# Kernel tuning notes

Hardware: AMD Instinct MI355X
Metric: run time of the kernel (lower is better)

## Reference

```python
import jax, jax.numpy as jnp
import numpy as np
from functools import partial

H, W = 96, 96                 # PNet output feature-map size
N = H * W                     # candidate boxes
STRIDE = 2.0
CELL = 12.0
SCALE = 12.0 / 20.0           # net_size / min_face_size (first pyramid level)
CLS_THR = 0.6
NMS_THR1 = 0.5                # per-scale NMS
NMS_THR2 = 0.7                # final NMS


def _iou_matrix(b):
    # b: [N,4] boxes (x1,y1,x2,y2); pixel convention with +1, eps as in source
    x1, y1, x2, y2 = b[:, 0], b[:, 1], b[:, 2], b[:, 3]
    area = (x2 - x1 + 1.0) * (y2 - y1 + 1.0)                      # [N]
    xx1 = jnp.maximum(x1[:, None], x1[None, :])
    yy1 = jnp.maximum(y1[:, None], y1[None, :])
    xx2 = jnp.minimum(x2[:, None], x2[None, :])
    yy2 = jnp.minimum(y2[:, None], y2[None, :])
    w = jnp.maximum(0.0, xx2 - xx1 + 1.0)
    h = jnp.maximum(0.0, yy2 - yy1 + 1.0)
    inter = w * h                                                  # [N,N]
    return inter / (area[:, None] + area[None, :] - inter + 1e-10)


def _greedy_nms(iou, valid, thr):
    # Sequential greedy suppression over score-sorted boxes (rows of iou).
    # A kept box suppresses all LOWER-ranked boxes with IoU > thr.
    n = valid.shape[0]
    ranks = jnp.arange(n)

    def step(suppressed, i):
        kept_i = valid[i] & (~suppressed[i])
        suppressed = suppressed | (kept_i & (iou[i] > thr) & (ranks > i))
        return suppressed, kept_i

    _, keep = jax.lax.scan(step, jnp.zeros(n, dtype=bool), ranks)
    return keep


def _forward(cls_map, reg):
    score = cls_map.reshape(-1)                                    # [N]
    dreg = reg.reshape(-1, 4)                                      # [N,4]
    ys, xs = jnp.meshgrid(jnp.arange(H, dtype=cls_map.dtype),
                          jnp.arange(W, dtype=cls_map.dtype), indexing='ij')
    x1 = jnp.round(STRIDE * xs / SCALE).reshape(-1)
    y1 = jnp.round(STRIDE * ys / SCALE).reshape(-1)
    x2 = jnp.round((STRIDE * xs + CELL) / SCALE).reshape(-1)
    y2 = jnp.round((STRIDE * ys + CELL) / SCALE).reshape(-1)
    boxes = jnp.stack([x1, y1, x2, y2], axis=1)                    # [N,4]

    order = jnp.argsort(-score)                                    # desc by score
    b = boxes[order]
    s = score[order]
    d = dreg[order]
    valid = s > CLS_THR                                            # threshold-gather as mask

    iou = _iou_matrix(b)                                           # [N,N] ~340MB
    keep = _greedy_nms(iou, valid, NMS_THR1)                       # per-scale NMS
    keep = _greedy_nms(iou, keep, NMS_THR2)                        # final NMS

    # box calibration (boxes_c in the source)
    bbw = b[:, 2] - b[:, 0] + 1.0
    bbh = b[:, 3] - b[:, 1] + 1.0
    boxes_c = jnp.stack([b[:, 0] + d[:, 0] * bbw,
                         b[:, 1] + d[:, 1] * bbh,
                         b[:, 2] + d[:, 2] * bbw,
                         b[:, 3] + d[:, 3] * bbh,
                         s], axis=1)                               # [N,5]
    return boxes_c * keep[:, None].astype(boxes_c.dtype)


def setup_inputs() -> dict:
    key = jax.random.key(0)
    k1, k2 = jax.random.split(key)
    cls_map = jax.random.uniform(k1, (H, W), dtype=jnp.float32)        # face prob channel
    reg = 0.1 * jax.random.normal(k2, (H, W, 4), dtype=jnp.float32)    # bbox offsets
    return {"cls_map": cls_map, "reg": reg}


def reference(cls_map, reg):
    return _forward(cls_map, reg)
```

## Files before the change

### kernel.cpp

```cpp
#include <hip/hip_runtime.h>
#include <stdint.h>

#define HH 96
#define WW 96
#define NN (HH*WW)
#define NW 192
#define NMT 24
#define MT 384
#define NKT 9


__device__ __forceinline__ int coord1(int a) { return (10 * a + 1) / 3; }

__device__ __forceinline__ unsigned long long shifted(unsigned long long A,
                                                      unsigned long long B,
                                                      int h, int dj) {
    const unsigned long long W0 = h ? B : A;
    if (dj == 0) return W0;
    if (dj > 0) {
        const unsigned long long Wr = h ? 0ULL : B;
        return (W0 >> dj) | (Wr << (64 - dj));
    }
    const int d = -dj;
    const unsigned long long Wl = h ? A : 0ULL;
    return (W0 << d) | (Wl >> (64 - d));
}

__global__ __launch_bounds__(1024, 1) void kA(const float* __restrict__ cls,
                                              unsigned int* __restrict__ rankp,
                                              unsigned long long* __restrict__ kw) {
    __shared__ __align__(16) float s[NN];
    __shared__ unsigned long long Hh[12][NW];
    __shared__ unsigned long long K[NW], D[NW];
    const int tid = threadIdx.x;
    const int bid = blockIdx.x;

    if (bid != 0) {
        const int rb = bid - 1;
        const int kt = rb % NKT, mt = rb / NKT;
        const int base = mt * MT;
        unsigned long long* sk = (unsigned long long*)s;
        if (tid < MT) {
            const int m = base + tid;
            sk[tid] = ((unsigned long long)__float_as_uint(cls[m]) << 14)
                    | (unsigned long long)(16383 - m);
        }
        __syncthreads();
        const int k = kt * 1024 + tid;
        const unsigned long long kk =
            ((unsigned long long)__float_as_uint(cls[k]) << 14)
          | (unsigned long long)(16383 - k);
        const ulonglong2* sk2 = (const ulonglong2*)sk;
        unsigned c0 = 0, c1 = 0;
        #pragma unroll 4
        for (int m2 = 0; m2 < MT / 2; ++m2) {
            const ulonglong2 v = sk2[m2];
            c0 += (v.x > kk);
            c1 += (v.y > kk);
        }
        rankp[mt * NN + k] = c0 + c1;
        return;
    }

    const int lane = tid & 63;
    const int wave = tid >> 6;
    const int offs_di[12] = {0,0, 0,0, -1,1, -2,2, -1,-1, 1,1};
    const int offs_dj[12] = {-1,1,-2,2,  0,0,  0,0, -1, 1,-1,1};
    for (int i = tid; i < NN/4; i += 1024)
        ((float4*)s)[i] = ((const float4*)cls)[i];
    __syncthreads();
    for (int it = 0; it < 12; ++it) {
        const int w = wave + (it << 4);
        const int row = w >> 1;
        const int col = ((w & 1) << 6) + lane;
        const bool incell = (col < WW);
        const int c = row * WW + col;
        const float sc = incell ? s[c] : 0.0f;
        const unsigned bc = __float_as_uint(sc);
        const int cm3 = col % 3, rm3 = row % 3;
        const unsigned long long dinit = __ballot(!incell || !(sc > 0.6f));
        if (lane == 0) { D[w] = dinit; K[w] = 0ULL; }
        #pragma unroll
        for (int e = 0; e < 12; ++e) {
            const int ii = row + offs_di[e], jj = col + offs_dj[e];
            bool geo;
            switch (e) {
                case 2:  geo = (cm3 == 1); break;
                case 3:  geo = (cm3 == 2); break;
                case 6:  geo = (rm3 == 1); break;
                case 7:  geo = (rm3 == 2); break;
                case 8:  geo = !(cm3 == 2 && rm3 == 2); break;
                case 9:  geo = !(cm3 == 1 && rm3 == 2); break;
                case 10: geo = !(cm3 == 2 && rm3 == 1); break;
                case 11: geo = !(cm3 == 1 && rm3 == 1); break;
                default: geo = true;
            }
            const bool tb = (e==0)|(e==2)|(e==4)|(e==6)|(e==8)|(e==9);
            bool hp = false;
            if (incell && geo && ii >= 0 && ii < HH && jj >= 0 && jj < WW) {
                const unsigned bv = __float_as_uint(s[ii * WW + jj]);
                hp = tb ? (bv >= bc) : (bv > bc);
            }
            const unsigned long long m = __ballot(hp);
            if (lane == 0) Hh[e][w] = m;
        }
    }
    __syncthreads();
    if (wave >= 3) return;

    volatile unsigned long long* vK = K;
    volatile unsigned long long* vD = D;
    const int w = tid;
    const int row = w >> 1, h = w & 1;
    unsigned long long Hr[12];
    #pragma unroll
    for (int e = 0; e < 12; ++e) Hr[e] = Hh[e][w];
    unsigned long long myK = K[w], myD = D[w];
    for (int iter = 0; iter < 4096; ++iter) {
        if (!~myD) break;
        unsigned long long DA[5], DB[5], KA[5], KB[5];
        #pragma unroll
        for (int q = 0; q < 5; ++q) {
            const int rr = row + q - 2;
            const bool ok = (rr >= 0) && (rr < HH);
            DA[q] = ok ? vD[rr*2]   : 0ULL;
            DB[q] = ok ? vD[rr*2+1] : 0ULL;
        }
        #pragma unroll
        for (int q = 0; q < 5; ++q) {
            const int rr = row + q - 2;
            const bool ok = (rr >= 0) && (rr < HH);
            KA[q] = ok ? vK[rr*2]   : 0ULL;
            KB[q] = ok ? vK[rr*2+1] : 0ULL;
        }
        unsigned long long supp = 0ULL, alldet = ~0ULL;
        #pragma unroll
        for (int e = 0; e < 12; ++e) {
            const int q = offs_di[e] + 2;
            const int dj = offs_dj[e];
            supp   |=  Hr[e] & shifted(KA[q], KB[q], h, dj);
            alldet &= ~Hr[e] | shifted(DA[q], DB[q], h, dj);
        }
        const unsigned long long U = ~myD;
        myK = myK | (U & alldet & ~supp);
        myD = myD | (U & (supp | alldet));
        vK[w] = myK;
        vD[w] = myD;
    }
    kw[w] = myK;
}

__global__ void kout(const float* __restrict__ score, const float* __restrict__ reg,
                     const unsigned int* __restrict__ rankp,
                     const unsigned long long* __restrict__ kw,
                     float* __restrict__ out) {
    const int k = blockIdx.x * 256 + threadIdx.x;
    unsigned r = 0;
    #pragma unroll
    for (int y = 0; y < NMT; ++y) r += rankp[y * NN + k];
    const int j = k % WW, i = k / WW;
    const bool kp = ((kw[i * 2 + (j >> 6)] >> (j & 63)) & 1ULL) != 0ULL;
    const float x1 = (float)coord1(j);
    const float y1 = (float)coord1(i);
    const float4 d = ((const float4*)reg)[k];
    float* o = out + (size_t)r * 5;
    o[0] = kp ? (x1 + d.x * 21.0f) : 0.0f;
    o[1] = kp ? (y1 + d.y * 21.0f) : 0.0f;
    o[2] = kp ? (x1 + 20.0f + d.z * 21.0f) : 0.0f;
    o[3] = kp ? (y1 + 20.0f + d.w * 21.0f) : 0.0f;
    o[4] = kp ? score[k] : 0.0f;
}

extern "C" void kernel_launch(void* const* d_in, const int* in_sizes, int n_in,
                              void* d_out, int out_size, void* d_ws, size_t ws_size,
                              hipStream_t stream) {
    const float* cls = (const float*)d_in[0];
    const float* reg = (const float*)d_in[1];
    float* out = (float*)d_out;
    char* ws = (char*)d_ws;
    unsigned int* rankp = (unsigned int*)(ws);
    unsigned long long* kw = (unsigned long long*)(ws + 884736);

    kA<<<217, 1024, 0, stream>>>(cls, rankp, kw);
    kout<<<36, 256, 0, stream>>>(cls, reg, rankp, kw, out);
}
```

Baseline: 80.94 us.

## Split fixpoint NMS by half-row with compile-time shifts and fewer LDS loads

```diff
diff --git a/kernel.cpp b/kernel.cpp
--- a/kernel.cpp
+++ b/kernel.cpp
@@ -12,18 +12,80 @@
 
 __device__ __forceinline__ int coord1(int a) { return (10 * a + 1) / 3; }
 
-__device__ __forceinline__ unsigned long long shifted(unsigned long long A,
-                                                      unsigned long long B,
-                                                      int h, int dj) {
-    const unsigned long long W0 = h ? B : A;
-    if (dj == 0) return W0;
-    if (dj > 0) {
-        const unsigned long long Wr = h ? 0ULL : B;
-        return (W0 >> dj) | (Wr << (64 - dj));
-    }
-    const int d = -dj;
-    const unsigned long long Wl = h ? A : 0ULL;
-    return (W0 << d) | (Wl >> (64 - d));
+template<int H, int DJ>
+__device__ __forceinline__ unsigned long long shf(unsigned long long S,
+                                                  unsigned long long O) {
+    if constexpr (DJ == 0) {
+        return S;
+    } else if constexpr (H == 0) {
+        if constexpr (DJ > 0) return (S >> DJ) | (O << (64 - DJ));
+        else                  return (S << (-DJ));
+    } else {
+        if constexpr (DJ > 0) return (S >> DJ);
+        else                  return (S << (-DJ)) | (O >> (64 + DJ));
+    }
+}
+
+template<int H>
+__device__ __forceinline__ unsigned long long runfix(
+    const int row, const unsigned long long (&Hr)[12],
+    volatile unsigned long long* vKs, volatile unsigned long long* vKo,
+    volatile unsigned long long* vDs, volatile unsigned long long* vDo,
+    unsigned long long myK, unsigned long long myD) {
+    const bool okm1 = row >= 1, okp1 = row <= HH - 2;
+    const bool okm2 = row >= 2, okp2 = row <= HH - 3;
+    for (int iter = 0; iter < 4096; ++iter) {
+        if (!~myD) break;
+        const unsigned long long D0o  = vDo[row];
+        const unsigned long long Dm1s = okm1 ? vDs[row-1] : 0ULL;
+        const unsigned long long Dm1o = okm1 ? vDo[row-1] : 0ULL;
+        const unsigned long long Dp1s = okp1 ? vDs[row+1] : 0ULL;
+        const unsigned long long Dp1o = okp1 ? vDo[row+1] : 0ULL;
+        const unsigned long long Dm2  = okm2 ? vDs[row-2] : 0ULL;
+        const unsigned long long Dp2  = okp2 ? vDs[row+2] : 0ULL;
+        const unsigned long long K0o  = vKo[row];
+        const unsigned long long Km1s = okm1 ? vKs[row-1] : 0ULL;
+        const unsigned long long Km1o = okm1 ? vKo[row-1] : 0ULL;
+        const unsigned long long Kp1s = okp1 ? vKs[row+1] : 0ULL;
+        const unsigned long long Kp1o = okp1 ? vKo[row+1] : 0ULL;
+        const unsigned long long Km2  = okm2 ? vKs[row-2] : 0ULL;
+        const unsigned long long Kp2  = okp2 ? vKs[row+2] : 0ULL;
+
+        unsigned long long supp = 0ULL;
+        supp |= Hr[0]  & shf<H,-1>(myK,  K0o);
+        supp |= Hr[1]  & shf<H,+1>(myK,  K0o);
+        supp |= Hr[2]  & shf<H,-2>(myK,  K0o);
+        supp |= Hr[3]  & shf<H,+2>(myK,  K0o);
+        supp |= Hr[4]  & Km1s;
+        supp |= Hr[5]  & Kp1s;
+        supp |= Hr[6]  & Km2;
+        supp |= Hr[7]  & Kp2;
+        supp |= Hr[8]  & shf<H,-1>(Km1s, Km1o);
+        supp |= Hr[9]  & shf<H,+1>(Km1s, Km1o);
+        supp |= Hr[10] & shf<H,-1>(Kp1s, Kp1o);
+        supp |= Hr[11] & shf<H,+1>(Kp1s, Kp1o);
+
+        unsigned long long alldet = ~0ULL;
+        alldet &= ~Hr[0]  | shf<H,-1>(myD,  D0o);
+        alldet &= ~Hr[1]  | shf<H,+1>(myD,  D0o);
+        alldet &= ~Hr[2]  | shf<H,-2>(myD,  D0o);
+        alldet &= ~Hr[3]  | shf<H,+2>(myD,  D0o);
+        alldet &= ~Hr[4]  | Dm1s;
+        alldet &= ~Hr[5]  | Dp1s;
+        alldet &= ~Hr[6]  | Dm2;
+        alldet &= ~Hr[7]  | Dp2;
+        alldet &= ~Hr[8]  | shf<H,-1>(Dm1s, Dm1o);
+        alldet &= ~Hr[9]  | shf<H,+1>(Dm1s, Dm1o);
+        alldet &= ~Hr[10] | shf<H,-1>(Dp1s, Dp1o);
+        alldet &= ~Hr[11] | shf<H,+1>(Dp1s, Dp1o);
+
+        const unsigned long long U = ~myD;
+        myK |= U & alldet & ~supp;
+        myD |= U & (supp | alldet);
+        vKs[row] = myK;
+        vDs[row] = myD;
+    }
+    return myK;
 }
 
 __global__ __launch_bounds__(1024, 1) void kA(const float* __restrict__ cls,
@@ -31,7 +93,7 @@
                                               unsigned long long* __restrict__ kw) {
     __shared__ __align__(16) float s[NN];
     __shared__ unsigned long long Hh[12][NW];
-    __shared__ unsigned long long K[NW], D[NW];
+    __shared__ unsigned long long K2[2][HH], D2[2][HH];
     const int tid = threadIdx.x;
     const int bid = blockIdx.x;
 
@@ -79,7 +141,7 @@
         const unsigned bc = __float_as_uint(sc);
         const int cm3 = col % 3, rm3 = row % 3;
         const unsigned long long dinit = __ballot(!incell || !(sc > 0.6f));
-        if (lane == 0) { D[w] = dinit; K[w] = 0ULL; }
+        if (lane == 0) { D2[w & 1][w >> 1] = dinit; K2[w & 1][w >> 1] = 0ULL; }
         #pragma unroll
         for (int e = 0; e < 12; ++e) {
             const int ii = row + offs_di[e], jj = col + offs_dj[e];
@@ -106,48 +168,27 @@
         }
     }
     __syncthreads();
-    if (wave >= 3) return;
-
-    volatile unsigned long long* vK = K;
-    volatile unsigned long long* vD = D;
-    const int w = tid;
-    const int row = w >> 1, h = w & 1;
+    if (wave >= 4 || lane >= 48) return;
+    const int h2 = wave >> 1;
+    const int row = ((wave & 1) * 48) + lane;
     unsigned long long Hr[12];
     #pragma unroll
-    for (int e = 0; e < 12; ++e) Hr[e] = Hh[e][w];
-    unsigned long long myK = K[w], myD = D[w];
-    for (int iter = 0; iter < 4096; ++iter) {
-        if (!~myD) break;
-        unsigned long long DA[5], DB[5], KA[5], KB[5];
-        #pragma unroll
-        for (int q = 0; q < 5; ++q) {
-            const int rr = row + q - 2;
-            const bool ok = (rr >= 0) && (rr < HH);
-            DA[q] = ok ? vD[rr*2]   : 0ULL;
-            DB[q] = ok ? vD[rr*2+1] : 0ULL;
-        }
-        #pragma unroll
-        for (int q = 0; q < 5; ++q) {
-            const int rr = row + q - 2;
-            const bool ok = (rr >= 0) && (rr < HH);
-            KA[q] = ok ? vK[rr*2]   : 0ULL;
-            KB[q] = ok ? vK[rr*2+1] : 0ULL;
-        }
-        unsigned long long supp = 0ULL, alldet = ~0ULL;
-        #pragma unroll
-        for (int e = 0; e < 12; ++e) {
-            const int q = offs_di[e] + 2;
-            const int dj = offs_dj[e];
-            supp   |=  Hr[e] & shifted(KA[q], KB[q], h, dj);
-            alldet &= ~Hr[e] | shifted(DA[q], DB[q], h, dj);
-        }
-        const unsigned long long U = ~myD;
-        myK = myK | (U & alldet & ~supp);
-        myD = myD | (U & (supp | alldet));
-        vK[w] = myK;
-        vD[w] = myD;
-    }
-    kw[w] = myK;
+    for (int e = 0; e < 12; ++e) Hr[e] = Hh[e][row * 2 + h2];
+    const unsigned long long myK = K2[h2][row], myD = D2[h2][row];
+    unsigned long long fin;
+    if (h2 == 0)
+        fin = runfix<0>(row, Hr,
+                        (volatile unsigned long long*)&K2[0][0],
+                        (volatile unsigned long long*)&K2[1][0],
+                        (volatile unsigned long long*)&D2[0][0],
+                        (volatile unsigned long long*)&D2[1][0], myK, myD);
+    else
+        fin = runfix<1>(row, Hr,
+                        (volatile unsigned long long*)&K2[1][0],
+                        (volatile unsigned long long*)&K2[0][0],
+                        (volatile unsigned long long*)&D2[1][0],
+                        (volatile unsigned long long*)&D2[0][0], myK, myD);
+    kw[row * 2 + h2] = fin;
 }
 
 __global__ void kout(const float* __restrict__ score, const float* __restrict__ reg,
```

Measured after the change: 79.47 us. About the same (-1.8%).
